# Optimization experiments

Measured on AMD Instinct MI355X. Metric: run time of the kernel, lower is better.

## Reference

```python
import jax, jax.numpy as jnp
import numpy as np

L, D, H, V, T_MAX, DFF = 8, 1024, 16, 50257, 1024, 4096
HS = D // H
EPS = 1e-5


def setup_inputs() -> dict:
    key = jax.random.key(0)
    ks = jax.random.split(key, 20)
    s = 0.02
    inp = {
        "idx": jax.random.randint(ks[0], (4, 1024), 0, V),
        "wte": jax.random.normal(ks[1], (V, D), jnp.float32) * s,
        "wpe": jax.random.normal(ks[2], (T_MAX, D), jnp.float32) * s,
        "wq": jax.random.normal(ks[3], (L, D, D), jnp.float32) * s,
        "wk": jax.random.normal(ks[4], (L, D, D), jnp.float32) * s,
        "wv": jax.random.normal(ks[5], (L, D, D), jnp.float32) * s,
        "wo": jax.random.normal(ks[6], (L, D, D), jnp.float32) * s,
        "bo": jnp.zeros((L, D), jnp.float32),
        "ln1_w": jnp.ones((L, D), jnp.float32),
        "ln1_b": jnp.zeros((L, D), jnp.float32),
        "ln2_w": jnp.ones((L, D), jnp.float32),
        "ln2_b": jnp.zeros((L, D), jnp.float32),
        "w1": jax.random.normal(ks[7], (L, D, DFF), jnp.float32) * s,
        "b1": jnp.zeros((L, DFF), jnp.float32),
        "w2": jax.random.normal(ks[8], (L, DFF, D), jnp.float32) * s,
        "b2": jnp.zeros((L, D), jnp.float32),
        "lnf_w": jnp.ones((D,), jnp.float32),
        "lnf_b": jnp.zeros((D,), jnp.float32),
        "wlm": jax.random.normal(ks[9], (D, V), jnp.float32) * s,
        "blm": jnp.zeros((V,), jnp.float32),
    }
    return inp


def _ln(x, w, b):
    mu = jnp.mean(x, axis=-1, keepdims=True)
    var = jnp.mean(jnp.square(x - mu), axis=-1, keepdims=True)
    return (x - mu) * jax.lax.rsqrt(var + EPS) * w + b


def _gpt_forward(idx, wte, wpe, wq, wk, wv, wo, bo, ln1_w, ln1_b, ln2_w, ln2_b,
                 w1, b1, w2, b2, lnf_w, lnf_b, wlm, blm):
    B, T = idx.shape
    x = wte[idx] + wpe[:T]                       # [B,T,D]
    causal = jnp.tril(jnp.ones((T, T), bool))    # same as tril buffer
    scale = HS ** -0.5
    for i in range(L):
        h = _ln(x, ln1_w[i], ln1_b[i])
        q = (h @ wq[i]).reshape(B, T, H, HS)
        k = (h @ wk[i]).reshape(B, T, H, HS)
        v = (h @ wv[i]).reshape(B, T, H, HS)
        wei = jnp.einsum('bqhd,bkhd->bhqk', q, k) * scale
        wei = jnp.where(causal, wei, -jnp.inf)
        wei = jax.nn.softmax(wei, axis=-1)
        attn = jnp.einsum('bhqk,bkhd->bqhd', wei, v).reshape(B, T, D)
        x = x + attn @ wo[i] + bo[i]
        h2 = _ln(x, ln2_w[i], ln2_b[i])
        x = x + jax.nn.relu(h2 @ w1[i] + b1[i]) @ w2[i] + b2[i]
    x = _ln(x, lnf_w, lnf_b)
    return x @ wlm + blm                          # logits [B,T,V]


def reference(idx, wte, wpe, wq, wk, wv, wo, bo, ln1_w, ln1_b, ln2_w, ln2_b,
              w1, b1, w2, b2, lnf_w, lnf_b, wlm, blm):
    return _gpt_forward(idx, wte, wpe, wq, wk, wv, wo, bo, ln1_w, ln1_b,
                        ln2_w, ln2_b, w1, b1, w2, b2, lnf_w, lnf_b, wlm, blm)
```

## Files before the change

kernel.cpp:

```cpp
#include <hip/hip_runtime.h>
#include <cstdint>
#include <cstddef>

typedef __attribute__((ext_vector_type(4))) float f32x4;
typedef __attribute__((ext_vector_type(8))) short s16x8;
typedef __attribute__((ext_vector_type(4))) unsigned short u16x4;
typedef __attribute__((ext_vector_type(2))) unsigned short u16x2;

#define NLAYER 8
#define DM 1024
#define NTOK 4096
#define DFF2 4096
#define NV 50257
#define NVPAD 50432

__device__ __forceinline__ unsigned short f2bf(float f) {
  unsigned int u = __float_as_uint(f);
  u = u + 0x7fffu + ((u >> 16) & 1u);
  return (unsigned short)(u >> 16);
}

__device__ __forceinline__ void gload_lds16(const void* gp, void* lp) {
  const __attribute__((address_space(1))) unsigned int* g =
      reinterpret_cast<const __attribute__((address_space(1))) unsigned int*>(
          reinterpret_cast<uintptr_t>(gp));
  __attribute__((address_space(3))) unsigned int* l =
      reinterpret_cast<__attribute__((address_space(3))) unsigned int*>(
          (unsigned int)(uintptr_t)lp);
  __builtin_amdgcn_global_load_lds(g, l, 16, 0, 0);
}

__global__ void __launch_bounds__(256) convT_k(const float* __restrict__ in,
                                               unsigned short* __restrict__ out,
                                               int K, int N, size_t zStride) {
  __shared__ float tile[64][65];
  const int n0 = blockIdx.x * 64, k0 = blockIdx.y * 64;
  const float* inp = in + (size_t)blockIdx.z * K * N;
  unsigned short* outp = out + (size_t)blockIdx.z * zStride;
  const int tid = threadIdx.x;
#pragma unroll
  for (int p = 0; p < 16; ++p) {
    const int r = p * 4 + (tid >> 6);
    const int cc = tid & 63;
    const int gn = n0 + cc;
    tile[r][cc] = (gn < N) ? inp[(size_t)(k0 + r) * N + gn] : 0.f;
  }
  __syncthreads();
#pragma unroll
  for (int p = 0; p < 8; ++p) {
    const int lin = p * 256 + tid;
    const int rn = lin >> 5;
    const int c2 = (lin & 31) * 2;
    u16x2 o;
    o[0] = f2bf(tile[c2][rn]);
    o[1] = f2bf(tile[c2 + 1][rn]);
    *(u16x2*)&outp[(size_t)(n0 + rn) * K + k0 + c2] = o;
  }
}

__global__ void __launch_bounds__(256) embed_k(const int* __restrict__ idx,
                                               const float* __restrict__ wte,
                                               const float* __restrict__ wpe,
                                               float* __restrict__ X) {
  const int tok = blockIdx.x;
  const int t = tok & 1023;
  const int id = idx[tok];
  const int c = threadIdx.x * 4;
  f32x4 a = *(const f32x4*)&wte[(size_t)id * DM + c];
  f32x4 p = *(const f32x4*)&wpe[(size_t)t * DM + c];
  a = a + p;
  *(f32x4*)&X[(size_t)tok * DM + c] = a;
}

__global__ void __launch_bounds__(256) ln_k(const float* __restrict__ X,
                                            const float* __restrict__ W,
                                            const float* __restrict__ Bp,
                                            unsigned short* __restrict__ O) {
  const int row = blockIdx.x, tid = threadIdx.x;
  const size_t base = (size_t)row * DM;
  f32x4 v = *(const f32x4*)&X[base + tid * 4];
  float s = v[0] + v[1] + v[2] + v[3];
  float q = v[0] * v[0] + v[1] * v[1] + v[2] * v[2] + v[3] * v[3];
#pragma unroll
  for (int m = 1; m < 64; m <<= 1) {
    s += __shfl_xor(s, m);
    q += __shfl_xor(q, m);
  }
  __shared__ float ps[4], pq[4];
  const int wv = tid >> 6;
  if ((tid & 63) == 0) { ps[wv] = s; pq[wv] = q; }
  __syncthreads();
  s = ps[0] + ps[1] + ps[2] + ps[3];
  q = pq[0] + pq[1] + pq[2] + pq[3];
  const float mu = s * (1.f / DM);
  const float var = q * (1.f / DM) - mu * mu;
  const float rstd = rsqrtf(var + 1e-5f);
  f32x4 w = *(const f32x4*)&W[tid * 4];
  f32x4 bb = *(const f32x4*)&Bp[tid * 4];
  u16x4 o;
#pragma unroll
  for (int j = 0; j < 4; ++j) o[j] = f2bf((v[j] - mu) * rstd * w[j] + bb[j]);
  *(u16x4*)&O[base + tid * 4] = o;
}

__global__ void __launch_bounds__(256) reduce2ln_k(
    float* __restrict__ X, const float* __restrict__ bias,
    const float* __restrict__ P0, const float* __restrict__ P1,
    const float* __restrict__ W, const float* __restrict__ Bp,
    unsigned short* __restrict__ O) {
  const int row = blockIdx.x, tid = threadIdx.x;
  const size_t base = (size_t)row * DM;
  const size_t i = base + tid * 4;
  f32x4 v = *(f32x4*)&X[i];
  {
    f32x4 b = *(const f32x4*)&bias[tid * 4];
    f32x4 a = *(const f32x4*)&P0[i];
    f32x4 c = *(const f32x4*)&P1[i];
    v = v + b + a + c;
    *(f32x4*)&X[i] = v;
  }
  float s = v[0] + v[1] + v[2] + v[3];
  float q = v[0] * v[0] + v[1] * v[1] + v[2] * v[2] + v[3] * v[3];
#pragma unroll
  for (int m = 1; m < 64; m <<= 1) {
    s += __shfl_xor(s, m);
    q += __shfl_xor(q, m);
  }
  __shared__ float ps[4], pq[4];
  const int wv = tid >> 6;
  if ((tid & 63) == 0) { ps[wv] = s; pq[wv] = q; }
  __syncthreads();
  s = ps[0] + ps[1] + ps[2] + ps[3];
  q = pq[0] + pq[1] + pq[2] + pq[3];
  const float mu = s * (1.f / DM);
  const float var = q * (1.f / DM) - mu * mu;
  const float rstd = rsqrtf(var + 1e-5f);
  f32x4 w = *(const f32x4*)&W[tid * 4];
  f32x4 bb = *(const f32x4*)&Bp[tid * 4];
  u16x4 o;
#pragma unroll
  for (int j = 0; j < 4; ++j) o[j] = f2bf((v[j] - mu) * rstd * w[j] + bb[j]);
  *(u16x4*)&O[base + tid * 4] = o;
}

__global__ void __launch_bounds__(256) gemm_k(
    const unsigned short* __restrict__ A, const unsigned short* __restrict__ Bt,
    const float* __restrict__ bias, float* __restrict__ outF,
    unsigned short* __restrict__ outB, int M, int N, int K, int lda, int ldc) {
  __shared__ __align__(16) unsigned short lA[128 * 64];
  __shared__ __align__(16) unsigned short lB[128 * 64];
  const int tid = threadIdx.x;
  const int wv = tid >> 6, lane = tid & 63;
  const int row0 = blockIdx.y * 128, col0 = blockIdx.x * 128;
  const int wr = wv >> 1, wc = wv & 1;

  const int z = blockIdx.z;
  A += (size_t)z * K;
  Bt += (size_t)z * K;
  if (gridDim.z > 1) outF += (size_t)z * M * ldc;

  f32x4 acc[4][4] = {};

  const int sRow = tid >> 3;
  const int sColSw = ((tid & 7) * 8) ^ ((sRow & 7) * 8);
  const unsigned short* gA = A + (size_t)(row0 + sRow) * lda + sColSw;
  const unsigned short* gB = Bt + (size_t)(col0 + sRow) * lda + sColSw;
  unsigned short* lAd = lA + tid * 8;
  unsigned short* lBd = lB + tid * 8;
  const size_t step32 = (size_t)32 * lda;

  const int rbase = lane & 15;
  const int kHi = (lane >> 4) * 8;
  const int kSw = (lane & 7) * 8;

  for (int kt = 0; kt < K; kt += 64) {
#pragma unroll
    for (int i = 0; i < 4; ++i) {
      gload_lds16(gA + kt + i * step32, lAd + i * 2048);
      gload_lds16(gB + kt + i * step32, lBd + i * 2048);
    }
    __syncthreads();
    s16x8 af[2][4], bfr[2][4];
#pragma unroll
    for (int kk = 0; kk < 2; ++kk) {
      const int kph = (kk * 32 + kHi) ^ kSw;
#pragma unroll
      for (int m = 0; m < 4; ++m)
        af[kk][m] = *(const s16x8*)&lA[(wr * 64 + m * 16 + rbase) * 64 + kph];
#pragma unroll
      for (int n = 0; n < 4; ++n)
        bfr[kk][n] = *(const s16x8*)&lB[(wc * 64 + n * 16 + rbase) * 64 + kph];
    }
#pragma unroll
    for (int kk = 0; kk < 2; ++kk)
#pragma unroll
      for (int m = 0; m < 4; ++m)
#pragma unroll
        for (int n = 0; n < 4; ++n)
          acc[m][n] = __builtin_amdgcn_mfma_f32_16x16x32_bf16(
              af[kk][m], bfr[kk][n], acc[m][n], 0, 0, 0);
    __syncthreads();
  }

  const int baseRow = row0 + wr * 64 + ((lane >> 4) * 4);
  const int baseCol = col0 + wc * 64 + (lane & 15);
#pragma unroll
  for (int m = 0; m < 4; ++m) {
#pragma unroll
    for (int n = 0; n < 4; ++n) {
      const int colc = baseCol + n * 16;
      if (colc < N) {
        const float bv = bias ? bias[colc] : 0.f;
        const int rowc0 = baseRow + m * 16;
#pragma unroll
        for (int r = 0; r < 4; ++r) {
          float v = acc[m][n][r] + bv;
          if (outF) outF[(size_t)(rowc0 + r) * ldc + colc] = v;
          if (outB) outB[(size_t)(rowc0 + r) * ldc + colc] = f2bf(v);
        }
      }
    }
  }
}

__global__ void __launch_bounds__(512, 2) gemm256p_k(
    const unsigned short* __restrict__ A, const unsigned short* __restrict__ Bt,
    const float* __restrict__ bias, float* __restrict__ outF,
    unsigned short* __restrict__ outB, unsigned short* __restrict__ vt,
    int M, int N, int K, int lda, int ldc, int relu) {
  __shared__ __align__(16) unsigned short lds[4][2][8192];
  const int tid = threadIdx.x;
  const int wv = tid >> 6, lane = tid & 63;
  const int row0 = blockIdx.y * 256, col0 = blockIdx.x * 256;
  const int wr = wv >> 2, wc = wv & 3;

  f32x4 acc[8][4] = {};

  const int sRow = tid >> 2;
  const int sCol = ((tid & 3) ^ ((tid >> 3) & 3)) * 8;
  const unsigned short* gA = A + (size_t)(row0 + sRow) * lda + sCol;
  const unsigned short* gB = Bt + (size_t)(col0 + sRow) * lda + sCol;
  const size_t step128 = (size_t)128 * lda;

  const int rbase = lane & 15;
  const int grp = ((lane >> 4) ^ ((lane >> 1) & 3)) * 8;

  const int nt = K >> 5;

#define STG(t, x, g)                                              \
  {                                                               \
    unsigned short* d = &lds[(t) & 3][x][tid * 8];                \
    gload_lds16((g) + (size_t)(t) * 32, d);                       \
    gload_lds16((g) + (size_t)(t) * 32 + step128, d + 4096);      \
  }

  STG(0, 0, gA); STG(0, 1, gB);
  STG(1, 0, gA); STG(1, 1, gB);
  STG(2, 0, gA); STG(2, 1, gB);
  asm volatile("s_waitcnt vmcnt(8)" ::: "memory");
  __builtin_amdgcn_s_barrier();

  for (int t = 0; t < nt; ++t) {
    const unsigned short* la = &lds[t & 3][0][0];
    const unsigned short* lb = &lds[t & 3][1][0];
    s16x8 bf[4], af[4];
#pragma unroll
    for (int n = 0; n < 4; ++n)
      bf[n] = *(const s16x8*)&lb[(wc * 64 + n * 16 + rbase) * 32 + grp];
#pragma unroll
    for (int m = 0; m < 4; ++m)
      af[m] = *(const s16x8*)&la[(wr * 128 + m * 16 + rbase) * 32 + grp];
    if (t + 3 < nt) STG(t + 3, 0, gA);
    __builtin_amdgcn_s_setprio(1);
#pragma unroll
    for (int m = 0; m < 4; ++m)
#pragma unroll
      for (int n = 0; n < 4; ++n)
        acc[m][n] = __builtin_amdgcn_mfma_f32_16x16x32_bf16(af[m], bf[n],
                                                            acc[m][n], 0, 0, 0);
    __builtin_amdgcn_s_setprio(0);
#pragma unroll
    for (int m = 0; m < 4; ++m)
      af[m] = *(const s16x8*)&la[(wr * 128 + 64 + m * 16 + rbase) * 32 + grp];
    if (t + 3 < nt) STG(t + 3, 1, gB);
    __builtin_amdgcn_s_setprio(1);
#pragma unroll
    for (int m = 0; m < 4; ++m)
#pragma unroll
      for (int n = 0; n < 4; ++n)
        acc[4 + m][n] = __builtin_amdgcn_mfma_f32_16x16x32_bf16(
            af[m], bf[n], acc[4 + m][n], 0, 0, 0);
    __builtin_amdgcn_s_setprio(0);
    if (t < nt - 4)
      asm volatile("s_waitcnt vmcnt(8)" ::: "memory");
    else if (t == nt - 4)
      asm volatile("s_waitcnt vmcnt(0)" ::: "memory");
    __builtin_amdgcn_s_barrier();
  }
#undef STG

  const int baseRow = row0 + wr * 128 + ((lane >> 4) * 4);
  const int baseCol = col0 + wc * 64 + (lane & 15);
#pragma unroll
  for (int m = 0; m < 8; ++m) {
#pragma unroll
    for (int n = 0; n < 4; ++n) {
      const int colc = baseCol + n * 16;
      if (colc < N) {
        const int rowc0 = baseRow + m * 16;
        if (vt && colc >= 2048) {
          const int f = colc - 2048;
          const int b = rowc0 >> 10, t0 = rowc0 & 1023;
          u16x4 o;
#pragma unroll
          for (int r = 0; r < 4; ++r) o[r] = f2bf(acc[m][n][r]);
          *(u16x4*)&vt[((size_t)((b << 4) + (f >> 6)) * 64 + (f & 63)) * 1024 + t0] = o;
        } else {
          const float bv = bias ? bias[colc] : 0.f;
#pragma unroll
          for (int r = 0; r < 4; ++r) {
            float v = acc[m][n][r] + bv;
            if (relu) v = fmaxf(v, 0.f);
            if (outF) outF[(size_t)(rowc0 + r) * ldc + colc] = v;
            if (outB) outB[(size_t)(rowc0 + r) * ldc + colc] = f2bf(v);
          }
        }
      }
    }
  }
}

__global__ void __launch_bounds__(256) attn_k(const unsigned short* __restrict__ Q,
                                              const unsigned short* __restrict__ Kb,
                                              const unsigned short* __restrict__ Vt,
                                              unsigned short* __restrict__ O,
                                              int ldq) {
  const int qt = blockIdx.x;
  const int bh = blockIdx.y;
  const int b = bh >> 4, h = bh & 15;
  const int tid = threadIdx.x, wv = tid >> 6, lane = tid & 63;
  const int g = lane >> 4, c = lane & 15;
  __shared__ __align__(16) unsigned short lP[4][16 * 64];
  const int qw0 = qt * 64 + wv * 16;
  s16x8 qf0, qf1;
  {
    const size_t qoff = ((size_t)(b * 1024 + qw0 + c)) * ldq + h * 64 + g * 8;
    qf0 = *(const s16x8*)&Q[qoff];
    qf1 = *(const s16x8*)&Q[qoff + 32];
  }
  f32x4 acc[4] = {};
  float mrun[4], lrun[4];
#pragma unroll
  for (int r = 0; r < 4; ++r) { mrun[r] = -1e30f; lrun[r] = 0.f; }

  for (int kt = 0; kt <= qt; ++kt) {
    f32x4 s[4] = {};
#pragma unroll
    for (int n = 0; n < 4; ++n) {
      const size_t koff = ((size_t)(b * 1024 + kt * 64 + n * 16 + c)) * ldq + h * 64 + g * 8;
      s16x8 k0 = *(const s16x8*)&Kb[koff];
      s16x8 k1 = *(const s16x8*)&Kb[koff + 32];
      s[n] = __builtin_amdgcn_mfma_f32_16x16x32_bf16(qf0, k0, s[n], 0, 0, 0);
      s[n] = __builtin_amdgcn_mfma_f32_16x16x32_bf16(qf1, k1, s[n], 0, 0, 0);
    }
    float p[4][4], mx[4] = {-1e30f, -1e30f, -1e30f, -1e30f};
#pragma unroll
    for (int n = 0; n < 4; ++n)
#pragma unroll
      for (int r = 0; r < 4; ++r) {
        const int qrow = qw0 + g * 4 + r;
        const int key = kt * 64 + n * 16 + c;
        float v = s[n][r] * 0.125f;
        if (key > qrow) v = -1e30f;
        p[n][r] = v;
        mx[r] = fmaxf(mx[r], v);
      }
#pragma unroll
    for (int r = 0; r < 4; ++r)
#pragma unroll
      for (int m = 1; m <= 8; m <<= 1) mx[r] = fmaxf(mx[r], __shfl_xor(mx[r], m));
    float al[4], rs[4];
#pragma unroll
    for (int r = 0; r < 4; ++r) {
      const float mn = fmaxf(mrun[r], mx[r]);
      al[r] = __expf(mrun[r] - mn);
      mrun[r] = mn;
      rs[r] = 0.f;
    }
#pragma unroll
    for (int n = 0; n < 4; ++n)
#pragma unroll
      for (int r = 0; r < 4; ++r) {
        const float e = __expf(p[n][r] - mrun[r]);
        p[n][r] = e;
        rs[r] += e;
      }
#pragma unroll
    for (int r = 0; r < 4; ++r) {
#pragma unroll
      for (int m = 1; m <= 8; m <<= 1) rs[r] += __shfl_xor(rs[r], m);
      lrun[r] = lrun[r] * al[r] + rs[r];
    }
#pragma unroll
    for (int n = 0; n < 4; ++n)
#pragma unroll
      for (int r = 0; r < 4; ++r) acc[n][r] *= al[r];
    __syncthreads();
#pragma unroll
    for (int n = 0; n < 4; ++n)
#pragma unroll
      for (int r = 0; r < 4; ++r)
        lP[wv][(g * 4 + r) * 64 + n * 16 + c] = f2bf(p[n][r]);
    __syncthreads();
    s16x8 pa0 = *(const s16x8*)&lP[wv][c * 64 + g * 8];
    s16x8 pa1 = *(const s16x8*)&lP[wv][c * 64 + 32 + g * 8];
#pragma unroll
    for (int n = 0; n < 4; ++n) {
      const size_t voff = ((size_t)(bh * 64 + n * 16 + c)) * 1024 + kt * 64 + g * 8;
      s16x8 v0 = *(const s16x8*)&Vt[voff];
      s16x8 v1 = *(const s16x8*)&Vt[voff + 32];
      acc[n] = __builtin_amdgcn_mfma_f32_16x16x32_bf16(pa0, v0, acc[n], 0, 0, 0);
      acc[n] = __builtin_amdgcn_mfma_f32_16x16x32_bf16(pa1, v1, acc[n], 0, 0, 0);
    }
  }
#pragma unroll
  for (int n = 0; n < 4; ++n)
#pragma unroll
    for (int r = 0; r < 4; ++r) {
      const size_t row = (size_t)(b * 1024 + qw0 + g * 4 + r);
      O[row * DM + h * 64 + n * 16 + c] = f2bf(acc[n][r] / lrun[r]);
    }
}

extern "C" void kernel_launch(void* const* d_in, const int* in_sizes, int n_in,
                              void* d_out, int out_size, void* d_ws, size_t ws_size,
                              hipStream_t stream) {
  const int* idx = (const int*)d_in[0];
  const float* wte = (const float*)d_in[1];
  const float* wpe = (const float*)d_in[2];
  const float* wq = (const float*)d_in[3];
  const float* wk = (const float*)d_in[4];
  const float* wv = (const float*)d_in[5];
  const float* wo = (const float*)d_in[6];
  const float* bo = (const float*)d_in[7];
  const float* ln1w = (const float*)d_in[8];
  const float* ln1b = (const float*)d_in[9];
  const float* ln2w = (const float*)d_in[10];
  const float* ln2b = (const float*)d_in[11];
  const float* w1 = (const float*)d_in[12];
  const float* b1 = (const float*)d_in[13];
  const float* w2 = (const float*)d_in[14];
  const float* b2 = (const float*)d_in[15];
  const float* lnfw = (const float*)d_in[16];
  const float* lnfb = (const float*)d_in[17];
  const float* wlm = (const float*)d_in[18];
  const float* blm = (const float*)d_in[19];
  float* out = (float*)d_out;

  char* ws = (char*)d_ws;
  size_t off = 0;
  auto alloc = [&](size_t bytes) -> void* {
    void* p = ws + off;
    off += (bytes + 255) & ~(size_t)255;
    return p;
  };
  unsigned short* wqkvT = (unsigned short*)alloc((size_t)NLAYER * 3072 * DM * 2);
  unsigned short* woT = (unsigned short*)alloc((size_t)NLAYER * DM * DM * 2);
  unsigned short* w1T = (unsigned short*)alloc((size_t)NLAYER * DM * DFF2 * 2);
  unsigned short* w2T = (unsigned short*)alloc((size_t)NLAYER * DM * DFF2 * 2);
  unsigned short* wlmT = w1T;
  float* X = (float*)alloc((size_t)NTOK * DM * 4);
  unsigned short* Hb = (unsigned short*)alloc((size_t)NTOK * DM * 2);
  char* uni = (char*)alloc((size_t)32 * 1024 * 1024);
  unsigned short* QKVb = (unsigned short*)uni;
  unsigned short* Ab = (unsigned short*)(uni + (size_t)24 * 1024 * 1024);
  float* P0 = (float*)uni;
  float* P1 = (float*)(uni + (size_t)16 * 1024 * 1024);
  unsigned short* VtB = (unsigned short*)alloc((size_t)NTOK * DM * 2);
  unsigned short* Mid = (unsigned short*)alloc((size_t)NTOK * DFF2 * 2);
  float* MidF = (float*)Mid;

  const size_t qkvStride = (size_t)3072 * DM;
  convT_k<<<dim3(16, 16, 8), 256, 0, stream>>>(wq, wqkvT, DM, DM, qkvStride);
  convT_k<<<dim3(16, 16, 8), 256, 0, stream>>>(wk, wqkvT + (size_t)1024 * DM, DM, DM, qkvStride);
  convT_k<<<dim3(16, 16, 8), 256, 0, stream>>>(wv, wqkvT + (size_t)2048 * DM, DM, DM, qkvStride);
  convT_k<<<dim3(16, 16, 8), 256, 0, stream>>>(wo, woT, DM, DM, (size_t)DM * DM);
  convT_k<<<dim3(64, 16, 8), 256, 0, stream>>>(w1, w1T, DM, DFF2, (size_t)DM * DFF2);
  convT_k<<<dim3(16, 64, 8), 256, 0, stream>>>(w2, w2T, DFF2, DM, (size_t)DM * DFF2);

  embed_k<<<dim3(NTOK), 256, 0, stream>>>(idx, wte, wpe, X);
  ln_k<<<dim3(NTOK), 256, 0, stream>>>(X, ln1w, ln1b, Hb);

  for (int i = 0; i < NLAYER; ++i) {
    const size_t wOff = (size_t)i * DM * DM;
    const size_t fOff = (size_t)i * DM * DFF2;
    gemm256p_k<<<dim3(12, 16), 512, 0, stream>>>(Hb, wqkvT + i * qkvStride,
                                                 nullptr, nullptr, QKVb, VtB,
                                                 NTOK, 3072, DM, DM, 3072, 0);
    attn_k<<<dim3(16, 64), 256, 0, stream>>>(QKVb, QKVb + 1024, VtB, Ab, 3072);
    gemm_k<<<dim3(8, 32, 2), 256, 0, stream>>>(Ab, woT + wOff, nullptr, MidF,
                                               nullptr, NTOK, DM, DM / 2, DM, DM);
    reduce2ln_k<<<dim3(NTOK), 256, 0, stream>>>(X, bo + i * DM, MidF,
                                                MidF + (size_t)NTOK * DM,
                                                ln2w + i * DM, ln2b + i * DM, Hb);
    gemm256p_k<<<dim3(16, 16), 512, 0, stream>>>(Hb, w1T + fOff, b1 + i * DFF2,
                                                 nullptr, Mid, nullptr, NTOK,
                                                 DFF2, DM, DM, DFF2, 1);
    gemm_k<<<dim3(8, 32, 2), 256, 0, stream>>>(Mid, w2T + fOff, nullptr, P0,
                                               nullptr, NTOK, DM, DFF2 / 2,
                                               DFF2, DM);
    const float* nw = (i < NLAYER - 1) ? ln1w + (i + 1) * DM : lnfw;
    const float* nb = (i < NLAYER - 1) ? ln1b + (i + 1) * DM : lnfb;
    reduce2ln_k<<<dim3(NTOK), 256, 0, stream>>>(X, b2 + i * DM, P0, P1, nw, nb, Hb);
  }

  convT_k<<<dim3(788, 16, 1), 256, 0, stream>>>(wlm, wlmT, DM, NV, 0);
  gemm256p_k<<<dim3(197, 16), 512, 0, stream>>>(Hb, wlmT, blm, out, nullptr,
                                                nullptr, NTOK, NV, DM, DM, NV, 0);
}
```

Before: 3.331 ms.

## Restructure 256x256 GEMM into 8-phase schedule with K=64 double-buffered tiles

Changes the big bf16 GEMM kernel from a 4-stage K=32 LDS ring to a 2-stage K=64 double buffer whose A and B halves live in separate buffers. Each iteration is split into four MFMA quadrants, and global-to-LDS loads and LDS reads are interleaved between barriers. An 8-way XOR swizzle is used for the wider rows. The aim is to raise MFMA density per barrier and spread memory traffic across the iteration, at the cost of more barriers and a shallower prefetch depth.

```diff
diff --git a/kernel.cpp b/kernel.cpp
--- a/kernel.cpp
+++ b/kernel.cpp
@@ -12,7 +12,6 @@
 #define NTOK 4096
 #define DFF2 4096
 #define NV 50257
-#define NVPAD 50432
 
 __device__ __forceinline__ unsigned short f2bf(float f) {
   unsigned int u = __float_as_uint(f);
@@ -223,12 +222,13 @@
   }
 }
 
-__global__ void __launch_bounds__(512, 2) gemm256p_k(
+__global__ void __launch_bounds__(512, 2) gemm8p_k(
     const unsigned short* __restrict__ A, const unsigned short* __restrict__ Bt,
     const float* __restrict__ bias, float* __restrict__ outF,
     unsigned short* __restrict__ outB, unsigned short* __restrict__ vt,
     int M, int N, int K, int lda, int ldc, int relu) {
-  __shared__ __align__(16) unsigned short lds[4][2][8192];
+  __shared__ __align__(16) unsigned short lA[2][2][8192];
+  __shared__ __align__(16) unsigned short lB[2][2][8192];
   const int tid = threadIdx.x;
   const int wv = tid >> 6, lane = tid & 63;
   const int row0 = blockIdx.y * 256, col0 = blockIdx.x * 256;
@@ -236,71 +236,129 @@
 
   f32x4 acc[8][4] = {};
 
-  const int sRow = tid >> 2;
-  const int sCol = ((tid & 3) ^ ((tid >> 3) & 3)) * 8;
-  const unsigned short* gA = A + (size_t)(row0 + sRow) * lda + sCol;
-  const unsigned short* gB = Bt + (size_t)(col0 + sRow) * lda + sCol;
-  const size_t step128 = (size_t)128 * lda;
+  const int sColSw = (((tid & 7) ^ ((tid >> 3) & 7))) * 8;
+  const unsigned short* gA = A + (size_t)(row0 + (tid >> 3)) * lda + sColSw;
+  const unsigned short* gB = Bt + (size_t)(col0 + (tid >> 3)) * lda + sColSw;
+  const size_t step64 = (size_t)64 * lda;
 
   const int rbase = lane & 15;
-  const int grp = ((lane >> 4) ^ ((lane >> 1) & 3)) * 8;
-
-  const int nt = K >> 5;
-
-#define STG(t, x, g)                                              \
-  {                                                               \
-    unsigned short* d = &lds[(t) & 3][x][tid * 8];                \
-    gload_lds16((g) + (size_t)(t) * 32, d);                       \
-    gload_lds16((g) + (size_t)(t) * 32 + step128, d + 4096);      \
-  }
-
-  STG(0, 0, gA); STG(0, 1, gB);
-  STG(1, 0, gA); STG(1, 1, gB);
-  STG(2, 0, gA); STG(2, 1, gB);
-  asm volatile("s_waitcnt vmcnt(8)" ::: "memory");
+  const int g8 = (lane >> 4) * 8;
+  const int rsw = (rbase & 7) * 8;
+
+  const int nt = K >> 6;
+
+#define STGA(t, h)                                                       \
+  {                                                                      \
+    const unsigned short* s_ = gA + (size_t)(t) * 64 + (size_t)(2 * (h)) * step64; \
+    gload_lds16(s_, &lA[(t) & 1][h][tid * 8]);                           \
+    gload_lds16(s_ + step64, &lA[(t) & 1][h][4096 + tid * 8]);           \
+  }
+#define STGB(t, h)                                                       \
+  {                                                                      \
+    const unsigned short* s_ = gB + (size_t)(t) * 64 + (size_t)(2 * (h)) * step64; \
+    gload_lds16(s_, &lB[(t) & 1][h][tid * 8]);                           \
+    gload_lds16(s_ + step64, &lB[(t) & 1][h][4096 + tid * 8]);           \
+  }
+
+  STGA(0, 0); STGA(0, 1); STGB(0, 0); STGB(0, 1);
+  STGA(1, 0); STGA(1, 1); STGB(1, 0);
+  asm volatile("s_waitcnt vmcnt(6)" ::: "memory");
   __builtin_amdgcn_s_barrier();
 
   for (int t = 0; t < nt; ++t) {
-    const unsigned short* la = &lds[t & 3][0][0];
-    const unsigned short* lb = &lds[t & 3][1][0];
-    s16x8 bf[4], af[4];
-#pragma unroll
-    for (int n = 0; n < 4; ++n)
-      bf[n] = *(const s16x8*)&lb[(wc * 64 + n * 16 + rbase) * 32 + grp];
+    const int d = t & 1;
+    const unsigned short* lah = &lA[d][wr][0];
+    const unsigned short* lbh = &lB[d][wc >> 1][0];
+    const int bro = (wc & 1) * 64;
+    s16x8 af0[4][2], af1[4][2], bf01[2][2], bf23[2][2];
+#pragma unroll
+    for (int ks = 0; ks < 2; ++ks) {
+      const int kph = (ks * 32 + g8) ^ rsw;
+#pragma unroll
+      for (int m = 0; m < 4; ++m)
+        af0[m][ks] = *(const s16x8*)&lah[(m * 16 + rbase) * 64 + kph];
+#pragma unroll
+      for (int n = 0; n < 2; ++n)
+        bf01[n][ks] = *(const s16x8*)&lbh[(bro + n * 16 + rbase) * 64 + kph];
+    }
+    if (t + 1 < nt) STGB(t + 1, 1);
+    __builtin_amdgcn_s_barrier();
+    asm volatile("s_waitcnt lgkmcnt(0)" ::: "memory");
+    __builtin_amdgcn_s_setprio(1);
 #pragma unroll
     for (int m = 0; m < 4; ++m)
-      af[m] = *(const s16x8*)&la[(wr * 128 + m * 16 + rbase) * 32 + grp];
-    if (t + 3 < nt) STG(t + 3, 0, gA);
+#pragma unroll
+      for (int n = 0; n < 2; ++n)
+#pragma unroll
+        for (int ks = 0; ks < 2; ++ks)
+          acc[m][n] = __builtin_amdgcn_mfma_f32_16x16x32_bf16(
+              af0[m][ks], bf01[n][ks], acc[m][n], 0, 0, 0);
+    __builtin_amdgcn_s_setprio(0);
+    __builtin_amdgcn_s_barrier();
+#pragma unroll
+    for (int ks = 0; ks < 2; ++ks) {
+      const int kph = (ks * 32 + g8) ^ rsw;
+#pragma unroll
+      for (int m = 0; m < 4; ++m)
+        af1[m][ks] = *(const s16x8*)&lah[(64 + m * 16 + rbase) * 64 + kph];
+    }
+    __builtin_amdgcn_s_barrier();
+    asm volatile("s_waitcnt lgkmcnt(0)" ::: "memory");
     __builtin_amdgcn_s_setprio(1);
 #pragma unroll
     for (int m = 0; m < 4; ++m)
 #pragma unroll
-      for (int n = 0; n < 4; ++n)
-        acc[m][n] = __builtin_amdgcn_mfma_f32_16x16x32_bf16(af[m], bf[n],
-                                                            acc[m][n], 0, 0, 0);
+      for (int n = 0; n < 2; ++n)
+#pragma unroll
+        for (int ks = 0; ks < 2; ++ks)
+          acc[4 + m][n] = __builtin_amdgcn_mfma_f32_16x16x32_bf16(
+              af1[m][ks], bf01[n][ks], acc[4 + m][n], 0, 0, 0);
     __builtin_amdgcn_s_setprio(0);
+    __builtin_amdgcn_s_barrier();
+#pragma unroll
+    for (int ks = 0; ks < 2; ++ks) {
+      const int kph = (ks * 32 + g8) ^ rsw;
+#pragma unroll
+      for (int n = 0; n < 2; ++n)
+        bf23[n][ks] =
+            *(const s16x8*)&lbh[(bro + 32 + n * 16 + rbase) * 64 + kph];
+    }
+    if (t + 2 < nt) STGA(t + 2, 0);
+    __builtin_amdgcn_s_barrier();
+    asm volatile("s_waitcnt lgkmcnt(0)" ::: "memory");
+    __builtin_amdgcn_s_setprio(1);
 #pragma unroll
     for (int m = 0; m < 4; ++m)
-      af[m] = *(const s16x8*)&la[(wr * 128 + 64 + m * 16 + rbase) * 32 + grp];
-    if (t + 3 < nt) STG(t + 3, 1, gB);
+#pragma unroll
+      for (int n = 0; n < 2; ++n)
+#pragma unroll
+        for (int ks = 0; ks < 2; ++ks)
+          acc[m][2 + n] = __builtin_amdgcn_mfma_f32_16x16x32_bf16(
+              af0[m][ks], bf23[n][ks], acc[m][2 + n], 0, 0, 0);
+    __builtin_amdgcn_s_setprio(0);
+    __builtin_amdgcn_s_barrier();
+    if (t + 2 < nt) { STGA(t + 2, 1); STGB(t + 2, 0); }
     __builtin_amdgcn_s_setprio(1);
 #pragma unroll
     for (int m = 0; m < 4; ++m)
 #pragma unroll
-      for (int n = 0; n < 4; ++n)
-        acc[4 + m][n] = __builtin_amdgcn_mfma_f32_16x16x32_bf16(
-            af[m], bf[n], acc[4 + m][n], 0, 0, 0);
+      for (int n = 0; n < 2; ++n)
+#pragma unroll
+        for (int ks = 0; ks < 2; ++ks)
+          acc[4 + m][2 + n] = __builtin_amdgcn_mfma_f32_16x16x32_bf16(
+              af1[m][ks], bf23[n][ks], acc[4 + m][2 + n], 0, 0, 0);
     __builtin_amdgcn_s_setprio(0);
-    if (t < nt - 4)
-      asm volatile("s_waitcnt vmcnt(8)" ::: "memory");
-    else if (t == nt - 4)
+    if (t + 2 < nt)
+      asm volatile("s_waitcnt vmcnt(6)" ::: "memory");
+    else if (t + 1 < nt)
       asm volatile("s_waitcnt vmcnt(0)" ::: "memory");
     __builtin_amdgcn_s_barrier();
   }
-#undef STG
+#undef STGA
+#undef STGB
 
   const int baseRow = row0 + wr * 128 + ((lane >> 4) * 4);
-  const int baseCol = col0 + wc * 64 + (lane & 15);
+  const int baseCol = col0 + wc * 64 + rbase;
 #pragma unroll
   for (int m = 0; m < 8; ++m) {
 #pragma unroll
@@ -494,18 +552,18 @@
   for (int i = 0; i < NLAYER; ++i) {
     const size_t wOff = (size_t)i * DM * DM;
     const size_t fOff = (size_t)i * DM * DFF2;
-    gemm256p_k<<<dim3(12, 16), 512, 0, stream>>>(Hb, wqkvT + i * qkvStride,
-                                                 nullptr, nullptr, QKVb, VtB,
-                                                 NTOK, 3072, DM, DM, 3072, 0);
+    gemm8p_k<<<dim3(12, 16), 512, 0, stream>>>(Hb, wqkvT + i * qkvStride,
+                                               nullptr, nullptr, QKVb, VtB,
+                                               NTOK, 3072, DM, DM, 3072, 0);
     attn_k<<<dim3(16, 64), 256, 0, stream>>>(QKVb, QKVb + 1024, VtB, Ab, 3072);
     gemm_k<<<dim3(8, 32, 2), 256, 0, stream>>>(Ab, woT + wOff, nullptr, MidF,
                                                nullptr, NTOK, DM, DM / 2, DM, DM);
     reduce2ln_k<<<dim3(NTOK), 256, 0, stream>>>(X, bo + i * DM, MidF,
                                                 MidF + (size_t)NTOK * DM,
                                                 ln2w + i * DM, ln2b + i * DM, Hb);
-    gemm256p_k<<<dim3(16, 16), 512, 0, stream>>>(Hb, w1T + fOff, b1 + i * DFF2,
-                                                 nullptr, Mid, nullptr, NTOK,
-                                                 DFF2, DM, DM, DFF2, 1);
+    gemm8p_k<<<dim3(16, 16), 512, 0, stream>>>(Hb, w1T + fOff, b1 + i * DFF2,
+                                               nullptr, Mid, nullptr, NTOK,
+                                               DFF2, DM, DM, DFF2, 1);
     gemm_k<<<dim3(8, 32, 2), 256, 0, stream>>>(Mid, w2T + fOff, nullptr, P0,
                                                nullptr, NTOK, DM, DFF2 / 2,
                                                DFF2, DM);
@@ -515,6 +573,6 @@
   }
 
   convT_k<<<dim3(788, 16, 1), 256, 0, stream>>>(wlm, wlmT, DM, NV, 0);
-  gemm256p_k<<<dim3(197, 16), 512, 0, stream>>>(Hb, wlmT, blm, out, nullptr,
-                                                nullptr, NTOK, NV, DM, DM, NV, 0);
-}
+  gemm8p_k<<<dim3(197, 16), 512, 0, stream>>>(Hb, wlmT, blm, out, nullptr,
+                                              nullptr, NTOK, NV, DM, DM, NV, 0);
+}
```

New measurement: 3.342 ms. No clear change (+0.3%).
